# Performance work log

Hardware: AMD Instinct MI355X
Metric: run time of the kernel (lower is better)

## Reference

```python
import jax, jax.numpy as jnp
import numpy as np

N = 1024      # num_nodes
E = 4096      # edges (before self-loops)
HEADS = 8
B = 32
T = 64
HL = 512      # lstm_hidden_size (LSTMCell)
HR = 64       # hid_dim_lstmrr (rainfall LSTM)


def setup_inputs() -> dict:
    key = jax.random.key(0)
    ks = jax.random.split(key, 20)
    rn = lambda i, shape, s=0.05: (jax.random.normal(ks[i], shape, jnp.float32) * s)
    return dict(
        rainfall=rn(0, (B, T, 1), 1.0),
        inflow=rn(1, (B, T, 1), 1.0),
        edge_index=jax.random.randint(ks[2], (2, E), 0, N),
        lstm_Wih=rn(3, (4 * HR, 1)), lstm_Whh=rn(4, (4 * HR, HR)),
        lstm_bih=jnp.zeros(4 * HR), lstm_bhh=jnp.zeros(4 * HR),
        fc_W=rn(5, (N, HR)), fc_b=jnp.zeros(N),
        g1_W=rn(6, (3, HEADS * 3)), g1_as=rn(7, (HEADS, 3)), g1_ad=rn(8, (HEADS, 3)), g1_b=jnp.zeros(HEADS * 3),
        g2_W=rn(9, (24, HEADS * 2)), g2_as=rn(10, (HEADS, 2)), g2_ad=rn(11, (HEADS, 2)), g2_b=jnp.zeros(2),
        cell_Wih=rn(12, (4 * HL, 2 * N)), cell_Whh=rn(13, (4 * HL, HL)),
        cell_bih=jnp.zeros(4 * HL), cell_bhh=jnp.zeros(4 * HL),
        ln_g=jnp.ones(HL), ln_b=jnp.zeros(HL),
        lin_W=rn(14, (2 * N, HL)), lin_b=jnp.zeros(2 * N),
    )


def _gat(h_in, W, a_s, a_d, bias, src, dst, heads, oc, concat):
    # PyG GATConv: shared lin for src/dst, per-head attention, edge softmax by dst.
    n = h_in.shape[0]
    h = (h_in @ W).reshape(n, heads, oc)                       # [N, H, oc]
    logit = jax.nn.leaky_relu(jnp.sum(h * a_s, -1)[src] + jnp.sum(h * a_d, -1)[dst], 0.2)  # [Etot, H]
    m = jax.ops.segment_max(logit, dst, num_segments=n)
    e = jnp.exp(logit - m[dst])
    denom = jax.ops.segment_sum(e, dst, num_segments=n)
    alpha = e / (denom[dst] + 1e-16)                           # [Etot, H]
    out = jax.ops.segment_sum(h[src] * alpha[:, :, None], dst, num_segments=n)
    out = out.reshape(n, heads * oc) if concat else out.mean(1)
    return out + bias, alpha


def reference(rainfall, inflow, lstm_Wih, lstm_Whh, lstm_bih, lstm_bhh, fc_W, fc_b,
              g1_W, g1_as, g1_ad, g1_b, g2_W, g2_as, g2_ad, g2_b,
              cell_Wih, cell_Whh, cell_bih, cell_bhh, ln_g, ln_b, lin_W, lin_b, edge_index):
    Bb, Tt, _ = rainfall.shape
    loops = jnp.arange(N, dtype=edge_index.dtype)
    src = jnp.concatenate([edge_index[0], loops])              # PyG adds self-loops
    dst = jnp.concatenate([edge_index[1], loops])

    # rainfall LSTM (batch_first), gates ordered i,f,g,o as in torch
    def lstm_step(carry, xt):
        h, c = carry
        g = xt @ lstm_Wih.T + h @ lstm_Whh.T + lstm_bih + lstm_bhh
        i, f, gg, o = jnp.split(g, 4, -1)
        c = jax.nn.sigmoid(f) * c + jax.nn.sigmoid(i) * jnp.tanh(gg)
        h = jax.nn.sigmoid(o) * jnp.tanh(c)
        return (h, c), h
    z = jnp.zeros((Bb, HR), rainfall.dtype)
    _, hs = jax.lax.scan(lstm_step, (z, z), rainfall.transpose(1, 0, 2))   # [T, B, HR]
    runoff = jax.nn.leaky_relu(hs @ fc_W.T + fc_b, 0.01)                   # [T, B, N]
    runoff = runoff.at[:, :, 753].add(inflow.transpose(1, 0, 2)[:, :, 0])

    gat1 = jax.vmap(lambda x: _gat(x, g1_W, g1_as, g1_ad, g1_b, src, dst, HEADS, 3, True))
    gat2 = jax.vmap(lambda x: _gat(x, g2_W, g2_as, g2_ad, g2_b, src, dst, HEADS, 2, False))

    def step(carry, r_t):
        hn, cn, xn = carry
        lateral = r_t[:, :, None]                              # [B, N, 1]
        x = jnp.concatenate([xn, lateral], -1)                 # [B, N, 3]
        x1, att = gat1(x)
        x1 = jax.nn.leaky_relu(x1, 0.01)
        x2, _ = gat2(x1)
        x2 = jax.nn.leaky_relu(x2, 0.01)
        xf = x2.reshape(Bb, 2 * N)
        g = xf @ cell_Wih.T + hn @ cell_Whh.T + cell_bih + cell_bhh
        i, f, gg, o = jnp.split(g, 4, -1)
        cn = jax.nn.sigmoid(f) * cn + jax.nn.sigmoid(i) * jnp.tanh(gg)
        hn = jax.nn.sigmoid(o) * jnp.tanh(cn)
        mu = hn.mean(-1, keepdims=True)
        var = ((hn - mu) ** 2).mean(-1, keepdims=True)
        hn = (hn - mu) / jnp.sqrt(var + 1e-5) * ln_g + ln_b
        xn_flat = jax.nn.softplus(hn @ lin_W.T + lin_b)        # [B, 2N]
        return (hn, cn, xn_flat.reshape(Bb, N, 2)), (xn_flat, lateral, att)

    hn0 = jnp.zeros((Bb, HL), rainfall.dtype)
    cn0 = jnp.zeros((Bb, HL), rainfall.dtype)
    xn0 = jnp.zeros((Bb, N, 2), rainfall.dtype)
    _, (pred, lat, att) = jax.lax.scan(step, (hn0, cn0, xn0), runoff)
    prediction = pred.transpose(1, 0, 2)                       # [B, T, 2N]
    Lateral = lat.transpose(1, 0, 2, 3)                        # [B, T, N, 1]
    return prediction, Lateral, att                            # att: [T, B, E+N, HEADS]
```

## Files before the change

### kernel.cpp

```cpp
#include <hip/hip_runtime.h>
#include <hip/hip_bf16.h>

#define BB 32
#define TT 64
#define NNODE 1024
#define EE 4096
#define NEDGE 5120
#define NHEAD 8
#define HLL 512
#define HRR 64
#define TWO_N 2048
#define KCELL 2560

__device__ __forceinline__ float sigmoidf_(float x){ return 1.f/(1.f+expf(-x)); }
__device__ __forceinline__ float leaky(float x, float s){ return x>0.f? x : s*x; }

__global__ __launch_bounds__(256) void k_lstm(
    const float* __restrict__ rain, const float* __restrict__ Wih,
    const float* __restrict__ Whh, const float* __restrict__ bih,
    const float* __restrict__ bhh, float* __restrict__ hs){
  int b = blockIdx.x;
  int j = threadIdx.x;
  __shared__ float h_lds[HRR];
  __shared__ float g_lds[4*HRR];
  float wh[HRR];
  #pragma unroll
  for(int k=0;k<HRR;k++) wh[k] = Whh[j*HRR+k];
  float wi = Wih[j];
  float bias = bih[j] + bhh[j];
  float c = 0.f;
  if(j < HRR) h_lds[j] = 0.f;
  __syncthreads();
  for(int t=0;t<TT;t++){
    float x = rain[b*TT+t];
    float g = fmaf(wi, x, bias);
    #pragma unroll
    for(int k=0;k<HRR;k++) g = fmaf(wh[k], h_lds[k], g);
    g_lds[j] = g;
    __syncthreads();
    if(j < HRR){
      c = sigmoidf_(g_lds[HRR+j])*c + sigmoidf_(g_lds[j])*tanhf(g_lds[2*HRR+j]);
      float h = sigmoidf_(g_lds[3*HRR+j])*tanhf(c);
      h_lds[j] = h;
      hs[(t*BB+b)*HRR + j] = h;
    }
    __syncthreads();
  }
}

__global__ __launch_bounds__(256) void k_runoff(
    const float* __restrict__ hs, const float* __restrict__ fcW,
    const float* __restrict__ fcb, const float* __restrict__ inflow,
    float* __restrict__ runoff, float* __restrict__ lat){
  int p = blockIdx.x;
  int q = p & 3; int tb = p >> 2; int t = tb >> 5; int b = tb & 31;
  int n = q*256 + threadIdx.x;
  __shared__ float hrow[HRR];
  if(threadIdx.x < HRR) hrow[threadIdx.x] = hs[(t*BB+b)*HRR + threadIdx.x];
  __syncthreads();
  const float* wrow = fcW + n*HRR;
  float a0=0.f,a1=0.f,a2=0.f,a3=0.f;
  #pragma unroll
  for(int k=0;k<HRR;k+=4){
    float4 w = *reinterpret_cast<const float4*>(wrow + k);
    a0 = fmaf(w.x, hrow[k+0], a0);
    a1 = fmaf(w.y, hrow[k+1], a1);
    a2 = fmaf(w.z, hrow[k+2], a2);
    a3 = fmaf(w.w, hrow[k+3], a3);
  }
  float acc = (a0+a1)+(a2+a3) + fcb[n];
  float r = leaky(acc, 0.01f);
  if(n == 753) r += inflow[b*TT + t];
  runoff[(t*BB+b)*NNODE + n] = r;
  lat[(size_t)(b*TT+t)*NNODE + n] = r;
}

__global__ __launch_bounds__(1024) void k_csr_off(const int* __restrict__ ei, int* __restrict__ off){
  __shared__ int deg[NNODE];
  __shared__ int scn[NNODE];
  int tid = threadIdx.x;
  deg[tid] = 1;
  __syncthreads();
  for(int e=tid; e<EE; e+=1024) atomicAdd(&deg[ei[EE+e]], 1);
  __syncthreads();
  scn[tid] = deg[tid];
  __syncthreads();
  for(int ofs=1; ofs<1024; ofs<<=1){
    int add = (tid>=ofs)? scn[tid-ofs] : 0;
    __syncthreads();
    scn[tid] += add;
    __syncthreads();
  }
  off[tid+1] = scn[tid];
  if(tid==0) off[0] = 0;
}

__global__ __launch_bounds__(1024) void k_csr_fill(const int* __restrict__ ei,
    const int* __restrict__ off, int* __restrict__ adjp){
  __shared__ int dstb[EE];
  int tid = threadIdx.x;
  for(int e=tid; e<EE; e+=1024) dstb[e] = ei[EE+e];
  __syncthreads();
  int e = blockIdx.x*1024 + tid;
  int myd = dstb[e];
  int rank = 0;
  for(int ep=0; ep<e; ep++) rank += (dstb[ep]==myd) ? 1 : 0;
  adjp[off[myd]+rank] = (ei[e] << 13) | e;
  if(blockIdx.x==0) adjp[off[tid+1]-1] = (tid << 13) | (EE + tid);
}

__global__ __launch_bounds__(256) void k_prep0(const float* __restrict__ runoff,
    const float* __restrict__ g1W, const float* __restrict__ g1as, const float* __restrict__ g1ad,
    float* __restrict__ h1, float* __restrict__ s1, float* __restrict__ d1){
  int idx = blockIdx.x*256 + threadIdx.x;
  int b = idx >> 10; int n = idx & 1023;
  float x2 = runoff[b*NNODE + n];
  float hv[24];
  size_t base = (size_t)b*NNODE + n;
  #pragma unroll
  for(int o=0;o<24;o++){
    hv[o] = x2*g1W[48+o];
    h1[base*24+o] = hv[o];
  }
  #pragma unroll
  for(int hd=0; hd<NHEAD; hd++){
    float s=0.f, d=0.f;
    #pragma unroll
    for(int c=0;c<3;c++){
      float v = hv[hd*3+c];
      s = fmaf(v, g1as[hd*3+c], s);
      d = fmaf(v, g1ad[hd*3+c], d);
    }
    s1[base*8+hd] = s; d1[base*8+hd] = d;
  }
}

__global__ __launch_bounds__(256) void k_gat1f(
    const int* __restrict__ adjp, const int* __restrict__ off,
    const float* __restrict__ h1, const float* __restrict__ s1, const float* __restrict__ d1,
    const float* __restrict__ g1b, const float* __restrict__ g2W,
    const float* __restrict__ g2as, const float* __restrict__ g2ad,
    float* __restrict__ h2, float* __restrict__ s2, float* __restrict__ d2,
    float* __restrict__ att, int t){
  int tid = threadIdx.x;
  int g = tid >> 3; int hd = tid & 7;
  int p = blockIdx.x*32 + g;
  int b = p >> 10; int n = p & 1023;
  __shared__ float ss[NNODE*NHEAD];
  __shared__ float x1buf[32][25];
  size_t bbase = (size_t)b*NNODE;
  for(int i=tid; i<NNODE*NHEAD; i+=256) ss[i] = s1[bbase*8 + i];
  __syncthreads();
  int o0 = off[n], o1 = off[n+1];
  float dn = d1[(bbase+n)*8+hd];
  float m = -1e30f, den = 0.f;
  for(int idx=o0; idx<o1; idx++){
    int pk = adjp[idx]; int s = pk >> 13;
    float lg = leaky(ss[s*8+hd] + dn, 0.2f);
    if(lg > m){ den *= expf(m - lg); m = lg; }
    den += expf(lg - m);
  }
  float inv = 1.f/(den + 1e-16f);
  float o_0=0.f, o_1=0.f, o_2=0.f;
  for(int idx=o0; idx<o1; idx++){
    int pk = adjp[idx]; int s = pk >> 13; int eid = pk & 8191;
    float lg = leaky(ss[s*8+hd] + dn, 0.2f);
    float al = expf(lg - m)*inv;
    att[((size_t)(t*BB+b)*NEDGE + eid)*NHEAD + hd] = al;
    const float* hr = h1 + (bbase+s)*24 + hd*3;
    o_0 = fmaf(hr[0], al, o_0);
    o_1 = fmaf(hr[1], al, o_1);
    o_2 = fmaf(hr[2], al, o_2);
  }
  x1buf[g][hd*3+0] = leaky(o_0 + g1b[hd*3+0], 0.01f);
  x1buf[g][hd*3+1] = leaky(o_1 + g1b[hd*3+1], 0.01f);
  x1buf[g][hd*3+2] = leaky(o_2 + g1b[hd*3+2], 0.01f);
  __syncthreads();
  float h2v0=0.f, h2v1=0.f;
  int oA = hd*2, oB = hd*2+1;
  #pragma unroll
  for(int k=0;k<24;k++){
    float xv = x1buf[g][k];
    h2v0 = fmaf(xv, g2W[k*16+oA], h2v0);
    h2v1 = fmaf(xv, g2W[k*16+oB], h2v1);
  }
  h2[(bbase+n)*16+oA] = h2v0;
  h2[(bbase+n)*16+oB] = h2v1;
  s2[(bbase+n)*8+hd] = h2v0*g2as[oA] + h2v1*g2as[oB];
  d2[(bbase+n)*8+hd] = h2v0*g2ad[oA] + h2v1*g2ad[oB];
}

__global__ __launch_bounds__(256) void k_gat2f(
    const int* __restrict__ adjp, const int* __restrict__ off,
    const float* __restrict__ h2, const float* __restrict__ s2, const float* __restrict__ d2,
    const float* __restrict__ g2b, float* __restrict__ xf){
  int tid = threadIdx.x;
  int g = tid >> 3; int hd = tid & 7;
  int p = blockIdx.x*32 + g;
  int b = p >> 10; int n = p & 1023;
  __shared__ float ss[NNODE*NHEAD];
  __shared__ float outbuf[32][17];
  size_t bbase = (size_t)b*NNODE;
  for(int i=tid; i<NNODE*NHEAD; i+=256) ss[i] = s2[bbase*8 + i];
  __syncthreads();
  int o0 = off[n], o1 = off[n+1];
  float dn = d2[(bbase+n)*8+hd];
  float m = -1e30f, den = 0.f;
  for(int idx=o0; idx<o1; idx++){
    int pk = adjp[idx]; int s = pk >> 13;
    float lg = leaky(ss[s*8+hd] + dn, 0.2f);
    if(lg > m){ den *= expf(m - lg); m = lg; }
    den += expf(lg - m);
  }
  float inv = 1.f/(den + 1e-16f);
  float o_0=0.f, o_1=0.f;
  for(int idx=o0; idx<o1; idx++){
    int pk = adjp[idx]; int s = pk >> 13;
    float lg = leaky(ss[s*8+hd] + dn, 0.2f);
    float al = expf(lg - m)*inv;
    const float* hr = h2 + (bbase+s)*16 + hd*2;
    o_0 = fmaf(hr[0], al, o_0);
    o_1 = fmaf(hr[1], al, o_1);
  }
  outbuf[g][hd*2+0] = o_0;
  outbuf[g][hd*2+1] = o_1;
  __syncthreads();
  if(hd < 2){
    float acc = 0.f;
    #pragma unroll
    for(int k=0;k<8;k++) acc += outbuf[g][k*2+hd];
    float v = leaky(acc*0.125f + g2b[hd], 0.01f);
    xf[b*TWO_N + n*2 + hd] = v;
  }
}

__global__ __launch_bounds__(256) void k_cell_gemm(const float* __restrict__ xf,
    const float* __restrict__ hn, const float* __restrict__ Wih, const float* __restrict__ Whh,
    float* __restrict__ g0, float* __restrict__ g1){
  __shared__ float xl[256*33];
  int bid = blockIdx.x;
  int half = bid >> 8; int jb = bid & 255;
  int tid = threadIdx.x;
  int jl = tid >> 5; int b = tid & 31;
  int j = jb*8 + jl;
  float a0=0.f,a1=0.f,a2=0.f,a3=0.f;
  int kbeg = half*1280, kend = kbeg + 1280;
  for(int k0=kbeg; k0<kend; k0+=256){
    if(k0 < TWO_N){
      for(int i=0;i<32;i++) xl[tid*33+i] = xf[i*TWO_N + k0 + tid];
    } else {
      for(int i=0;i<32;i++) xl[tid*33+i] = hn[i*HLL + (k0-TWO_N) + tid];
    }
    __syncthreads();
    const float* wrow = (k0 < TWO_N) ? (Wih + (size_t)j*TWO_N + k0)
                                     : (Whh + (size_t)j*HLL + (k0-TWO_N));
    #pragma unroll 4
    for(int kk=0; kk<256; kk+=8){
      float4 w0 = *reinterpret_cast<const float4*>(wrow + kk);
      float4 w1 = *reinterpret_cast<const float4*>(wrow + kk + 4);
      const float* xp = &xl[kk*33 + b];
      a0 = fmaf(w0.x, xp[0*33], a0);
      a1 = fmaf(w0.y, xp[1*33], a1);
      a2 = fmaf(w0.z, xp[2*33], a2);
      a3 = fmaf(w0.w, xp[3*33], a3);
      a0 = fmaf(w1.x, xp[4*33], a0);
      a1 = fmaf(w1.y, xp[5*33], a1);
      a2 = fmaf(w1.z, xp[6*33], a2);
      a3 = fmaf(w1.w, xp[7*33], a3);
    }
    __syncthreads();
  }
  float* dst = half ? g1 : g0;
  dst[b*TWO_N + j] = (a0+a1)+(a2+a3);
}

__global__ __launch_bounds__(512) void k_cell_gate(const float* __restrict__ g0,
    const float* __restrict__ g1,
    const float* __restrict__ bih, const float* __restrict__ bhh,
    float* __restrict__ cn, float* __restrict__ hn,
    const float* __restrict__ lng, const float* __restrict__ lnb){
  int b = blockIdx.x; int u = threadIdx.x;
  const float* r0 = g0 + b*TWO_N;
  const float* r1 = g1 + b*TWO_N;
  float gi = r0[u]         + r1[u]         + bih[u]         + bhh[u];
  float gf = r0[HLL+u]     + r1[HLL+u]     + bih[HLL+u]     + bhh[HLL+u];
  float gg = r0[2*HLL+u]   + r1[2*HLL+u]   + bih[2*HLL+u]   + bhh[2*HLL+u];
  float go = r0[3*HLL+u]   + r1[3*HLL+u]   + bih[3*HLL+u]   + bhh[3*HLL+u];
  float c = sigmoidf_(gf)*cn[b*HLL+u] + sigmoidf_(gi)*tanhf(gg);
  cn[b*HLL+u] = c;
  float h = sigmoidf_(go)*tanhf(c);
  __shared__ float red[HLL];
  __shared__ float red2[HLL];
  red[u] = h; red2[u] = h*h;
  __syncthreads();
  for(int s=256; s>0; s>>=1){
    if(u < s){ red[u] += red[u+s]; red2[u] += red2[u+s]; }
    __syncthreads();
  }
  float mu = red[0] * (1.f/HLL);
  float var = red2[0] * (1.f/HLL) - mu*mu;
  float rstd = rsqrtf(var + 1e-5f);
  hn[b*HLL+u] = (h-mu)*rstd*lng[u] + lnb[u];
}

__global__ __launch_bounds__(256) void k_lin(const float* __restrict__ hn,
    const float* __restrict__ W, const float* __restrict__ bias,
    const float* __restrict__ runoff, float* __restrict__ pred,
    float* __restrict__ h1, float* __restrict__ s1, float* __restrict__ d1,
    const float* __restrict__ g1W, const float* __restrict__ g1as, const float* __restrict__ g1ad,
    int t){
  __shared__ float hl[256*33];
  int tid = threadIdx.x;
  int jl = tid >> 5; int b = tid & 31;
  int j = blockIdx.x*8 + jl;
  float a0=0.f,a1=0.f,a2=0.f,a3=0.f;
  for(int k0=0; k0<HLL; k0+=256){
    for(int i=0;i<32;i++) hl[tid*33+i] = hn[i*HLL + k0 + tid];
    __syncthreads();
    const float* wrow = W + (size_t)j*HLL + k0;
    #pragma unroll 4
    for(int kk=0; kk<256; kk+=8){
      float4 w0 = *reinterpret_cast<const float4*>(wrow + kk);
      float4 w1 = *reinterpret_cast<const float4*>(wrow + kk + 4);
      const float* xp = &hl[kk*33 + b];
      a0 = fmaf(w0.x, xp[0*33], a0);
      a1 = fmaf(w0.y, xp[1*33], a1);
      a2 = fmaf(w0.z, xp[2*33], a2);
      a3 = fmaf(w0.w, xp[3*33], a3);
      a0 = fmaf(w1.x, xp[4*33], a0);
      a1 = fmaf(w1.y, xp[5*33], a1);
      a2 = fmaf(w1.z, xp[6*33], a2);
      a3 = fmaf(w1.w, xp[7*33], a3);
    }
    __syncthreads();
  }
  float val = (a0+a1)+(a2+a3) + bias[j];
  float sp = fmaxf(val, 0.f) + log1pf(expf(-fabsf(val)));
  pred[((size_t)b*TT + t)*TWO_N + j] = sp;
  if(t+1 < TT){
    float partner = __shfl_xor(sp, 32);
    if((jl & 1) == 0){
      int n = j >> 1;
      float x2 = runoff[(size_t)(t+1)*BB*NNODE + b*NNODE + n];
      float hv[24];
      size_t base = (size_t)b*NNODE + n;
      #pragma unroll
      for(int o=0;o<24;o++){
        hv[o] = sp*g1W[o] + partner*g1W[24+o] + x2*g1W[48+o];
        h1[base*24+o] = hv[o];
      }
      #pragma unroll
      for(int hd=0; hd<NHEAD; hd++){
        float s=0.f, d=0.f;
        #pragma unroll
        for(int c=0;c<3;c++){
          float v = hv[hd*3+c];
          s = fmaf(v, g1as[hd*3+c], s);
          d = fmaf(v, g1ad[hd*3+c], d);
        }
        s1[base*8+hd] = s; d1[base*8+hd] = d;
      }
    }
  }
}

__global__ __launch_bounds__(512) void k_init(float* __restrict__ hn, float* __restrict__ cn){
  int idx = blockIdx.x*512 + threadIdx.x;
  if(idx < BB*HLL) hn[idx] = 0.f;
  else cn[idx - BB*HLL] = 0.f;
}

extern "C" void kernel_launch(void* const* d_in, const int* in_sizes, int n_in,
                              void* d_out, int out_size, void* d_ws, size_t ws_size,
                              hipStream_t stream){
  const float* rainfall  = (const float*)d_in[0];
  const float* inflow    = (const float*)d_in[1];
  const int*   edge_index= (const int*)  d_in[2];
  const float* lstm_Wih  = (const float*)d_in[3];
  const float* lstm_Whh  = (const float*)d_in[4];
  const float* lstm_bih  = (const float*)d_in[5];
  const float* lstm_bhh  = (const float*)d_in[6];
  const float* fc_W      = (const float*)d_in[7];
  const float* fc_b      = (const float*)d_in[8];
  const float* g1_W      = (const float*)d_in[9];
  const float* g1_as     = (const float*)d_in[10];
  const float* g1_ad     = (const float*)d_in[11];
  const float* g1_b      = (const float*)d_in[12];
  const float* g2_W      = (const float*)d_in[13];
  const float* g2_as     = (const float*)d_in[14];
  const float* g2_ad     = (const float*)d_in[15];
  const float* g2_b      = (const float*)d_in[16];
  const float* cell_Wih  = (const float*)d_in[17];
  const float* cell_Whh  = (const float*)d_in[18];
  const float* cell_bih  = (const float*)d_in[19];
  const float* cell_bhh  = (const float*)d_in[20];
  const float* ln_g      = (const float*)d_in[21];
  const float* ln_b      = (const float*)d_in[22];
  const float* lin_W     = (const float*)d_in[23];
  const float* lin_b     = (const float*)d_in[24];

  float* out  = (float*)d_out;
  float* pred = out;
  float* lat  = out + (size_t)4194304;
  float* att  = out + (size_t)6291456;

  float* ws = (float*)d_ws;
  float* hs     = ws;
  float* runoff = hs + 131072;
  float* h1     = runoff + 2097152;
  float* s1     = h1 + 786432;
  float* d1     = s1 + 262144;
  float* h2     = d1 + 262144;
  float* s2     = h2 + 524288;
  float* d2     = s2 + 262144;
  float* xfb    = d2 + 262144;
  float* g0buf  = xfb + 65536;
  float* g1buf  = g0buf + 65536;
  float* hn     = g1buf + 65536;
  float* cn     = hn + 16384;
  int*   off    = (int*)(cn + 16384);
  int*   adjp   = off + 1032;
  if(ws_size < 19292192ull) return;

  k_init<<<64, 512, 0, stream>>>(hn, cn);
  k_csr_off<<<1, 1024, 0, stream>>>(edge_index, off);
  k_csr_fill<<<4, 1024, 0, stream>>>(edge_index, off, adjp);
  k_lstm<<<BB, 256, 0, stream>>>(rainfall, lstm_Wih, lstm_Whh, lstm_bih, lstm_bhh, hs);
  k_runoff<<<TT*BB*4, 256, 0, stream>>>(hs, fc_W, fc_b, inflow, runoff, lat);
  k_prep0<<<128, 256, 0, stream>>>(runoff, g1_W, g1_as, g1_ad, h1, s1, d1);

  for(int t=0; t<TT; t++){
    k_gat1f<<<1024, 256, 0, stream>>>(adjp, off, h1, s1, d1,
        g1_b, g2_W, g2_as, g2_ad, h2, s2, d2, att, t);
    k_gat2f<<<1024, 256, 0, stream>>>(adjp, off, h2, s2, d2, g2_b, xfb);
    k_cell_gemm<<<512, 256, 0, stream>>>(xfb, hn, cell_Wih, cell_Whh, g0buf, g1buf);
    k_cell_gate<<<BB, 512, 0, stream>>>(g0buf, g1buf, cell_bih, cell_bhh, cn, hn, ln_g, ln_b);
    k_lin<<<256, 256, 0, stream>>>(hn, lin_W, lin_b, runoff, pred,
        h1, s1, d1, g1_W, g1_as, g1_ad, t);
  }
}
```

Baseline: 5.196 ms.

## Fuse both GAT layers into one per-batch kernel with LDS-resident node features

Replaces the separate gat1 and gat2 kernels, the prep kernel and the GAT-input precompute in k_lin with a single kernel that launches one 1024-thread block per batch row. The block keeps node inputs, layer-2 features and attention scores in LDS, recomputes layer-1 projections on the fly from the three raw inputs, and writes attention rows as float4. This removes global round-trips for the h1/s1/d1/h2/s2/d2 intermediates and one launch per timestep. In exchange only 32 blocks run per step, so parallelism across the GPU's compute units drops sharply and each thread handles all heads serially.

```diff
diff --git a/kernel.cpp b/kernel.cpp
--- a/kernel.cpp
+++ b/kernel.cpp
@@ -15,6 +15,40 @@
 __device__ __forceinline__ float sigmoidf_(float x){ return 1.f/(1.f+expf(-x)); }
 __device__ __forceinline__ float leaky(float x, float s){ return x>0.f? x : s*x; }
 
+__global__ __launch_bounds__(1024) void k_csr_off(const int* __restrict__ ei, int* __restrict__ off){
+  __shared__ int deg[NNODE];
+  __shared__ int scn[NNODE];
+  int tid = threadIdx.x;
+  deg[tid] = 1;
+  __syncthreads();
+  for(int e=tid; e<EE; e+=1024) atomicAdd(&deg[ei[EE+e]], 1);
+  __syncthreads();
+  scn[tid] = deg[tid];
+  __syncthreads();
+  for(int ofs=1; ofs<1024; ofs<<=1){
+    int add = (tid>=ofs)? scn[tid-ofs] : 0;
+    __syncthreads();
+    scn[tid] += add;
+    __syncthreads();
+  }
+  off[tid+1] = scn[tid];
+  if(tid==0) off[0] = 0;
+}
+
+__global__ __launch_bounds__(1024) void k_csr_fill(const int* __restrict__ ei,
+    const int* __restrict__ off, int* __restrict__ adjp){
+  __shared__ int dstb[EE];
+  int tid = threadIdx.x;
+  for(int e=tid; e<EE; e+=1024) dstb[e] = ei[EE+e];
+  __syncthreads();
+  int e = blockIdx.x*1024 + tid;
+  int myd = dstb[e];
+  int rank = 0;
+  for(int ep=0; ep<e; ep++) rank += (dstb[ep]==myd) ? 1 : 0;
+  adjp[off[myd]+rank] = (ei[e] << 13) | e;
+  if(blockIdx.x==0) adjp[off[tid+1]-1] = (tid << 13) | (EE + tid);
+}
+
 __global__ __launch_bounds__(256) void k_lstm(
     const float* __restrict__ rain, const float* __restrict__ Wih,
     const float* __restrict__ Whh, const float* __restrict__ bih,
@@ -59,7 +93,7 @@
   if(threadIdx.x < HRR) hrow[threadIdx.x] = hs[(t*BB+b)*HRR + threadIdx.x];
   __syncthreads();
   const float* wrow = fcW + n*HRR;
-  float a0=0.f,a1=0.f,a2=0.f,a3=0.f;
+  float a0=0,a1=0,a2=0,a3=0;
   #pragma unroll
   for(int k=0;k<HRR;k+=4){
     float4 w = *reinterpret_cast<const float4*>(wrow + k);
@@ -75,162 +109,148 @@
   lat[(size_t)(b*TT+t)*NNODE + n] = r;
 }
 
-__global__ __launch_bounds__(1024) void k_csr_off(const int* __restrict__ ei, int* __restrict__ off){
-  __shared__ int deg[NNODE];
-  __shared__ int scn[NNODE];
-  int tid = threadIdx.x;
-  deg[tid] = 1;
-  __syncthreads();
-  for(int e=tid; e<EE; e+=1024) atomicAdd(&deg[ei[EE+e]], 1);
-  __syncthreads();
-  scn[tid] = deg[tid];
-  __syncthreads();
-  for(int ofs=1; ofs<1024; ofs<<=1){
-    int add = (tid>=ofs)? scn[tid-ofs] : 0;
-    __syncthreads();
-    scn[tid] += add;
-    __syncthreads();
-  }
-  off[tid+1] = scn[tid];
-  if(tid==0) off[0] = 0;
-}
-
-__global__ __launch_bounds__(1024) void k_csr_fill(const int* __restrict__ ei,
-    const int* __restrict__ off, int* __restrict__ adjp){
-  __shared__ int dstb[EE];
-  int tid = threadIdx.x;
-  for(int e=tid; e<EE; e+=1024) dstb[e] = ei[EE+e];
-  __syncthreads();
-  int e = blockIdx.x*1024 + tid;
-  int myd = dstb[e];
-  int rank = 0;
-  for(int ep=0; ep<e; ep++) rank += (dstb[ep]==myd) ? 1 : 0;
-  adjp[off[myd]+rank] = (ei[e] << 13) | e;
-  if(blockIdx.x==0) adjp[off[tid+1]-1] = (tid << 13) | (EE + tid);
-}
-
-__global__ __launch_bounds__(256) void k_prep0(const float* __restrict__ runoff,
-    const float* __restrict__ g1W, const float* __restrict__ g1as, const float* __restrict__ g1ad,
-    float* __restrict__ h1, float* __restrict__ s1, float* __restrict__ d1){
-  int idx = blockIdx.x*256 + threadIdx.x;
-  int b = idx >> 10; int n = idx & 1023;
-  float x2 = runoff[b*NNODE + n];
-  float hv[24];
-  size_t base = (size_t)b*NNODE + n;
-  #pragma unroll
-  for(int o=0;o<24;o++){
-    hv[o] = x2*g1W[48+o];
-    h1[base*24+o] = hv[o];
-  }
-  #pragma unroll
-  for(int hd=0; hd<NHEAD; hd++){
-    float s=0.f, d=0.f;
-    #pragma unroll
-    for(int c=0;c<3;c++){
-      float v = hv[hd*3+c];
-      s = fmaf(v, g1as[hd*3+c], s);
-      d = fmaf(v, g1ad[hd*3+c], d);
-    }
-    s1[base*8+hd] = s; d1[base*8+hd] = d;
-  }
-}
-
-__global__ __launch_bounds__(256) void k_gat1f(
+__global__ __launch_bounds__(1024) void k_gat(
     const int* __restrict__ adjp, const int* __restrict__ off,
-    const float* __restrict__ h1, const float* __restrict__ s1, const float* __restrict__ d1,
-    const float* __restrict__ g1b, const float* __restrict__ g2W,
-    const float* __restrict__ g2as, const float* __restrict__ g2ad,
-    float* __restrict__ h2, float* __restrict__ s2, float* __restrict__ d2,
-    float* __restrict__ att, int t){
-  int tid = threadIdx.x;
-  int g = tid >> 3; int hd = tid & 7;
-  int p = blockIdx.x*32 + g;
-  int b = p >> 10; int n = p & 1023;
-  __shared__ float ss[NNODE*NHEAD];
-  __shared__ float x1buf[32][25];
-  size_t bbase = (size_t)b*NNODE;
-  for(int i=tid; i<NNODE*NHEAD; i+=256) ss[i] = s1[bbase*8 + i];
-  __syncthreads();
+    const float* __restrict__ xn, const float* __restrict__ runoff,
+    const float* __restrict__ g1W, const float* __restrict__ g1as,
+    const float* __restrict__ g1ad, const float* __restrict__ g1b,
+    const float* __restrict__ g2W, const float* __restrict__ g2as,
+    const float* __restrict__ g2ad, const float* __restrict__ g2b,
+    float* __restrict__ xf, float* __restrict__ att, int t){
+  __shared__ float SA[NNODE*24];
+  __shared__ float SB[NNODE*8];
+  __shared__ float SC[640];
+  const int tid = threadIdx.x;
+  const int b = blockIdx.x;
+  const int n = tid;
+
+  if(tid < 72)  SC[48+tid]  = g1W[tid];
+  if(tid >= 128 && tid < 512) SC[tid] = g2W[tid-128];
+  if(tid >= 512 && tid < 528) SC[tid] = g2as[tid-512];
+  if(tid >= 528 && tid < 544) SC[tid] = g2ad[tid-528];
+  if(tid >= 544 && tid < 546) SC[tid] = g2b[tid-544];
+  if(tid >= 552 && tid < 576) SC[tid] = g1b[tid-552];
+  if(tid >= 576 && tid < 600){
+    int i = tid-576; int hd = i/3, c = i%3;
+    float s=0,d=0;
+    #pragma unroll
+    for(int cc=0;cc<3;cc++){
+      float w = g1W[c*24+hd*3+cc];
+      s = fmaf(w, g1as[hd*3+cc], s);
+      d = fmaf(w, g1ad[hd*3+cc], d);
+    }
+    SC[i] = s; SC[24+i] = d;
+  }
+  float x0=0.f, x1v=0.f;
+  if(t > 0){ x0 = xn[b*TWO_N+2*n]; x1v = xn[b*TWO_N+2*n+1]; }
+  float x2 = runoff[((size_t)t*BB+b)*NNODE + n];
+  SB[n*3+0]=x0; SB[n*3+1]=x1v; SB[n*3+2]=x2;
+  __syncthreads();
+
   int o0 = off[n], o1 = off[n+1];
-  float dn = d1[(bbase+n)*8+hd];
-  float m = -1e30f, den = 0.f;
-  for(int idx=o0; idx<o1; idx++){
-    int pk = adjp[idx]; int s = pk >> 13;
-    float lg = leaky(ss[s*8+hd] + dn, 0.2f);
-    if(lg > m){ den *= expf(m - lg); m = lg; }
-    den += expf(lg - m);
-  }
-  float inv = 1.f/(den + 1e-16f);
-  float o_0=0.f, o_1=0.f, o_2=0.f;
-  for(int idx=o0; idx<o1; idx++){
-    int pk = adjp[idx]; int s = pk >> 13; int eid = pk & 8191;
-    float lg = leaky(ss[s*8+hd] + dn, 0.2f);
-    float al = expf(lg - m)*inv;
-    att[((size_t)(t*BB+b)*NEDGE + eid)*NHEAD + hd] = al;
-    const float* hr = h1 + (bbase+s)*24 + hd*3;
-    o_0 = fmaf(hr[0], al, o_0);
-    o_1 = fmaf(hr[1], al, o_1);
-    o_2 = fmaf(hr[2], al, o_2);
-  }
-  x1buf[g][hd*3+0] = leaky(o_0 + g1b[hd*3+0], 0.01f);
-  x1buf[g][hd*3+1] = leaky(o_1 + g1b[hd*3+1], 0.01f);
-  x1buf[g][hd*3+2] = leaky(o_2 + g1b[hd*3+2], 0.01f);
-  __syncthreads();
-  float h2v0=0.f, h2v1=0.f;
-  int oA = hd*2, oB = hd*2+1;
+  float m1[8], den1[8], dn1[8];
+  #pragma unroll
+  for(int h=0;h<8;h++){
+    m1[h] = -1e30f; den1[h] = 0.f;
+    dn1[h] = x0*SC[24+h*3+0] + x1v*SC[24+h*3+1] + x2*SC[24+h*3+2];
+  }
+  for(int e=o0;e<o1;e++){
+    int s = adjp[e]>>13;
+    float sx0=SB[s*3], sx1=SB[s*3+1], sx2=SB[s*3+2];
+    #pragma unroll
+    for(int h=0;h<8;h++){
+      float s1 = sx0*SC[h*3+0] + sx1*SC[h*3+1] + sx2*SC[h*3+2];
+      float lg = leaky(s1+dn1[h], 0.2f);
+      if(lg > m1[h]){ den1[h] *= expf(m1[h]-lg); m1[h] = lg; }
+      den1[h] += expf(lg-m1[h]);
+    }
+  }
+  float inv1[8];
+  #pragma unroll
+  for(int h=0;h<8;h++) inv1[h] = 1.f/(den1[h]+1e-16f);
+  float agg[24];
+  #pragma unroll
+  for(int k=0;k<24;k++) agg[k]=0.f;
+  for(int e=o0;e<o1;e++){
+    int pk = adjp[e]; int s = pk>>13; int eid = pk & 8191;
+    float sx0=SB[s*3], sx1=SB[s*3+1], sx2=SB[s*3+2];
+    float at8[8];
+    #pragma unroll
+    for(int h=0;h<8;h++){
+      float s1 = sx0*SC[h*3+0] + sx1*SC[h*3+1] + sx2*SC[h*3+2];
+      float lg = leaky(s1+dn1[h], 0.2f);
+      float al = expf(lg-m1[h])*inv1[h];
+      at8[h] = al;
+      #pragma unroll
+      for(int cc=0;cc<3;cc++){
+        float h1v = sx0*SC[48+h*3+cc] + sx1*SC[48+24+h*3+cc] + sx2*SC[48+48+h*3+cc];
+        agg[h*3+cc] = fmaf(al, h1v, agg[h*3+cc]);
+      }
+    }
+    float* ap = att + ((size_t)(t*BB+b)*NEDGE + eid)*NHEAD;
+    *reinterpret_cast<float4*>(ap)   = make_float4(at8[0],at8[1],at8[2],at8[3]);
+    *reinterpret_cast<float4*>(ap+4) = make_float4(at8[4],at8[5],at8[6],at8[7]);
+  }
+  float x1r[24];
   #pragma unroll
   for(int k=0;k<24;k++){
-    float xv = x1buf[g][k];
-    h2v0 = fmaf(xv, g2W[k*16+oA], h2v0);
-    h2v1 = fmaf(xv, g2W[k*16+oB], h2v1);
-  }
-  h2[(bbase+n)*16+oA] = h2v0;
-  h2[(bbase+n)*16+oB] = h2v1;
-  s2[(bbase+n)*8+hd] = h2v0*g2as[oA] + h2v1*g2as[oB];
-  d2[(bbase+n)*8+hd] = h2v0*g2ad[oA] + h2v1*g2ad[oB];
-}
-
-__global__ __launch_bounds__(256) void k_gat2f(
-    const int* __restrict__ adjp, const int* __restrict__ off,
-    const float* __restrict__ h2, const float* __restrict__ s2, const float* __restrict__ d2,
-    const float* __restrict__ g2b, float* __restrict__ xf){
-  int tid = threadIdx.x;
-  int g = tid >> 3; int hd = tid & 7;
-  int p = blockIdx.x*32 + g;
-  int b = p >> 10; int n = p & 1023;
-  __shared__ float ss[NNODE*NHEAD];
-  __shared__ float outbuf[32][17];
-  size_t bbase = (size_t)b*NNODE;
-  for(int i=tid; i<NNODE*NHEAD; i+=256) ss[i] = s2[bbase*8 + i];
-  __syncthreads();
-  int o0 = off[n], o1 = off[n+1];
-  float dn = d2[(bbase+n)*8+hd];
-  float m = -1e30f, den = 0.f;
-  for(int idx=o0; idx<o1; idx++){
-    int pk = adjp[idx]; int s = pk >> 13;
-    float lg = leaky(ss[s*8+hd] + dn, 0.2f);
-    if(lg > m){ den *= expf(m - lg); m = lg; }
-    den += expf(lg - m);
-  }
-  float inv = 1.f/(den + 1e-16f);
-  float o_0=0.f, o_1=0.f;
-  for(int idx=o0; idx<o1; idx++){
-    int pk = adjp[idx]; int s = pk >> 13;
-    float lg = leaky(ss[s*8+hd] + dn, 0.2f);
-    float al = expf(lg - m)*inv;
-    const float* hr = h2 + (bbase+s)*16 + hd*2;
-    o_0 = fmaf(hr[0], al, o_0);
-    o_1 = fmaf(hr[1], al, o_1);
-  }
-  outbuf[g][hd*2+0] = o_0;
-  outbuf[g][hd*2+1] = o_1;
-  __syncthreads();
-  if(hd < 2){
-    float acc = 0.f;
-    #pragma unroll
-    for(int k=0;k<8;k++) acc += outbuf[g][k*2+hd];
-    float v = leaky(acc*0.125f + g2b[hd], 0.01f);
-    xf[b*TWO_N + n*2 + hd] = v;
+    x1r[k] = leaky(agg[k] + SC[552+k], 0.01f);
+  }
+  __syncthreads();
+
+  float h2r[16];
+  #pragma unroll
+  for(int j=0;j<16;j++) h2r[j]=0.f;
+  #pragma unroll
+  for(int k=0;k<24;k++){
+    float xv = x1r[k];
+    #pragma unroll
+    for(int j=0;j<16;j++) h2r[j] = fmaf(xv, SC[128+k*16+j], h2r[j]);
+  }
+  float d2[8];
+  #pragma unroll
+  for(int h=0;h<8;h++){
+    SB[n*8+h] = h2r[2*h]*SC[512+2*h] + h2r[2*h+1]*SC[512+2*h+1];
+    d2[h]     = h2r[2*h]*SC[528+2*h] + h2r[2*h+1]*SC[528+2*h+1];
+  }
+  #pragma unroll
+  for(int j=0;j<16;j++) SA[n*16+j] = h2r[j];
+  __syncthreads();
+
+  float m2[8], den2[8];
+  #pragma unroll
+  for(int h=0;h<8;h++){ m2[h]=-1e30f; den2[h]=0.f; }
+  for(int e=o0;e<o1;e++){
+    int s = adjp[e]>>13;
+    #pragma unroll
+    for(int h=0;h<8;h++){
+      float lg = leaky(SB[s*8+h]+d2[h], 0.2f);
+      if(lg > m2[h]){ den2[h] *= expf(m2[h]-lg); m2[h] = lg; }
+      den2[h] += expf(lg-m2[h]);
+    }
+  }
+  float inv2[8];
+  #pragma unroll
+  for(int h=0;h<8;h++) inv2[h] = 1.f/(den2[h]+1e-16f);
+  float agg2[16];
+  #pragma unroll
+  for(int j=0;j<16;j++) agg2[j]=0.f;
+  for(int e=o0;e<o1;e++){
+    int s = adjp[e]>>13;
+    #pragma unroll
+    for(int h=0;h<8;h++){
+      float lg = leaky(SB[s*8+h]+d2[h], 0.2f);
+      float al = expf(lg-m2[h])*inv2[h];
+      agg2[2*h]   = fmaf(al, SA[s*16+2*h],   agg2[2*h]);
+      agg2[2*h+1] = fmaf(al, SA[s*16+2*h+1], agg2[2*h+1]);
+    }
+  }
+  #pragma unroll
+  for(int cc=0;cc<2;cc++){
+    float acc=0.f;
+    #pragma unroll
+    for(int h=0;h<8;h++) acc += agg2[2*h+cc];
+    xf[b*TWO_N + n*2 + cc] = leaky(acc*0.125f + SC[544+cc], 0.01f);
   }
 }
 
@@ -259,14 +279,14 @@
       float4 w0 = *reinterpret_cast<const float4*>(wrow + kk);
       float4 w1 = *reinterpret_cast<const float4*>(wrow + kk + 4);
       const float* xp = &xl[kk*33 + b];
-      a0 = fmaf(w0.x, xp[0*33], a0);
-      a1 = fmaf(w0.y, xp[1*33], a1);
-      a2 = fmaf(w0.z, xp[2*33], a2);
-      a3 = fmaf(w0.w, xp[3*33], a3);
-      a0 = fmaf(w1.x, xp[4*33], a0);
-      a1 = fmaf(w1.y, xp[5*33], a1);
-      a2 = fmaf(w1.z, xp[6*33], a2);
-      a3 = fmaf(w1.w, xp[7*33], a3);
+      a0 = fmaf(w0.x, xp[0],   a0);
+      a1 = fmaf(w0.y, xp[33],  a1);
+      a2 = fmaf(w0.z, xp[66],  a2);
+      a3 = fmaf(w0.w, xp[99],  a3);
+      a0 = fmaf(w1.x, xp[132], a0);
+      a1 = fmaf(w1.y, xp[165], a1);
+      a2 = fmaf(w1.z, xp[198], a2);
+      a3 = fmaf(w1.w, xp[231], a3);
     }
     __syncthreads();
   }
@@ -274,7 +294,7 @@
   dst[b*TWO_N + j] = (a0+a1)+(a2+a3);
 }
 
-__global__ __launch_bounds__(512) void k_cell_gate(const float* __restrict__ g0,
+__global__ __launch_bounds__(512) void k_gateln(const float* __restrict__ g0,
     const float* __restrict__ g1,
     const float* __restrict__ bih, const float* __restrict__ bhh,
     float* __restrict__ cn, float* __restrict__ hn,
@@ -282,10 +302,10 @@
   int b = blockIdx.x; int u = threadIdx.x;
   const float* r0 = g0 + b*TWO_N;
   const float* r1 = g1 + b*TWO_N;
-  float gi = r0[u]         + r1[u]         + bih[u]         + bhh[u];
-  float gf = r0[HLL+u]     + r1[HLL+u]     + bih[HLL+u]     + bhh[HLL+u];
-  float gg = r0[2*HLL+u]   + r1[2*HLL+u]   + bih[2*HLL+u]   + bhh[2*HLL+u];
-  float go = r0[3*HLL+u]   + r1[3*HLL+u]   + bih[3*HLL+u]   + bhh[3*HLL+u];
+  float gi = r0[u]       + r1[u]       + bih[u]       + bhh[u];
+  float gf = r0[HLL+u]   + r1[HLL+u]   + bih[HLL+u]   + bhh[HLL+u];
+  float gg = r0[2*HLL+u] + r1[2*HLL+u] + bih[2*HLL+u] + bhh[2*HLL+u];
+  float go = r0[3*HLL+u] + r1[3*HLL+u] + bih[3*HLL+u] + bhh[3*HLL+u];
   float c = sigmoidf_(gf)*cn[b*HLL+u] + sigmoidf_(gi)*tanhf(gg);
   cn[b*HLL+u] = c;
   float h = sigmoidf_(go)*tanhf(c);
@@ -305,10 +325,7 @@
 
 __global__ __launch_bounds__(256) void k_lin(const float* __restrict__ hn,
     const float* __restrict__ W, const float* __restrict__ bias,
-    const float* __restrict__ runoff, float* __restrict__ pred,
-    float* __restrict__ h1, float* __restrict__ s1, float* __restrict__ d1,
-    const float* __restrict__ g1W, const float* __restrict__ g1as, const float* __restrict__ g1ad,
-    int t){
+    float* __restrict__ pred, float* __restrict__ xn, int t){
   __shared__ float hl[256*33];
   int tid = threadIdx.x;
   int jl = tid >> 5; int b = tid & 31;
@@ -323,45 +340,21 @@
       float4 w0 = *reinterpret_cast<const float4*>(wrow + kk);
       float4 w1 = *reinterpret_cast<const float4*>(wrow + kk + 4);
       const float* xp = &hl[kk*33 + b];
-      a0 = fmaf(w0.x, xp[0*33], a0);
-      a1 = fmaf(w0.y, xp[1*33], a1);
-      a2 = fmaf(w0.z, xp[2*33], a2);
-      a3 = fmaf(w0.w, xp[3*33], a3);
-      a0 = fmaf(w1.x, xp[4*33], a0);
-      a1 = fmaf(w1.y, xp[5*33], a1);
-      a2 = fmaf(w1.z, xp[6*33], a2);
-      a3 = fmaf(w1.w, xp[7*33], a3);
+      a0 = fmaf(w0.x, xp[0],   a0);
+      a1 = fmaf(w0.y, xp[33],  a1);
+      a2 = fmaf(w0.z, xp[66],  a2);
+      a3 = fmaf(w0.w, xp[99],  a3);
+      a0 = fmaf(w1.x, xp[132], a0);
+      a1 = fmaf(w1.y, xp[165], a1);
+      a2 = fmaf(w1.z, xp[198], a2);
+      a3 = fmaf(w1.w, xp[231], a3);
     }
     __syncthreads();
   }
   float val = (a0+a1)+(a2+a3) + bias[j];
   float sp = fmaxf(val, 0.f) + log1pf(expf(-fabsf(val)));
   pred[((size_t)b*TT + t)*TWO_N + j] = sp;
-  if(t+1 < TT){
-    float partner = __shfl_xor(sp, 32);
-    if((jl & 1) == 0){
-      int n = j >> 1;
-      float x2 = runoff[(size_t)(t+1)*BB*NNODE + b*NNODE + n];
-      float hv[24];
-      size_t base = (size_t)b*NNODE + n;
-      #pragma unroll
-      for(int o=0;o<24;o++){
-        hv[o] = sp*g1W[o] + partner*g1W[24+o] + x2*g1W[48+o];
-        h1[base*24+o] = hv[o];
-      }
-      #pragma unroll
-      for(int hd=0; hd<NHEAD; hd++){
-        float s=0.f, d=0.f;
-        #pragma unroll
-        for(int c=0;c<3;c++){
-          float v = hv[hd*3+c];
-          s = fmaf(v, g1as[hd*3+c], s);
-          d = fmaf(v, g1ad[hd*3+c], d);
-        }
-        s1[base*8+hd] = s; d1[base*8+hd] = d;
-      }
-    }
-  }
+  xn[b*TWO_N + j] = sp;
 }
 
 __global__ __launch_bounds__(512) void k_init(float* __restrict__ hn, float* __restrict__ cn){
@@ -407,35 +400,27 @@
   float* ws = (float*)d_ws;
   float* hs     = ws;
   float* runoff = hs + 131072;
-  float* h1     = runoff + 2097152;
-  float* s1     = h1 + 786432;
-  float* d1     = s1 + 262144;
-  float* h2     = d1 + 262144;
-  float* s2     = h2 + 524288;
-  float* d2     = s2 + 262144;
-  float* xfb    = d2 + 262144;
+  float* xnb    = runoff + 2097152;
+  float* xfb    = xnb + 65536;
   float* g0buf  = xfb + 65536;
   float* g1buf  = g0buf + 65536;
   float* hn     = g1buf + 65536;
   float* cn     = hn + 16384;
   int*   off    = (int*)(cn + 16384);
   int*   adjp   = off + 1032;
-  if(ws_size < 19292192ull) return;
+  if(ws_size < 10117152ull) return;
 
   k_init<<<64, 512, 0, stream>>>(hn, cn);
   k_csr_off<<<1, 1024, 0, stream>>>(edge_index, off);
   k_csr_fill<<<4, 1024, 0, stream>>>(edge_index, off, adjp);
   k_lstm<<<BB, 256, 0, stream>>>(rainfall, lstm_Wih, lstm_Whh, lstm_bih, lstm_bhh, hs);
   k_runoff<<<TT*BB*4, 256, 0, stream>>>(hs, fc_W, fc_b, inflow, runoff, lat);
-  k_prep0<<<128, 256, 0, stream>>>(runoff, g1_W, g1_as, g1_ad, h1, s1, d1);
 
   for(int t=0; t<TT; t++){
-    k_gat1f<<<1024, 256, 0, stream>>>(adjp, off, h1, s1, d1,
-        g1_b, g2_W, g2_as, g2_ad, h2, s2, d2, att, t);
-    k_gat2f<<<1024, 256, 0, stream>>>(adjp, off, h2, s2, d2, g2_b, xfb);
+    k_gat<<<BB, 1024, 0, stream>>>(adjp, off, xnb, runoff,
+        g1_W, g1_as, g1_ad, g1_b, g2_W, g2_as, g2_ad, g2_b, xfb, att, t);
     k_cell_gemm<<<512, 256, 0, stream>>>(xfb, hn, cell_Wih, cell_Whh, g0buf, g1buf);
-    k_cell_gate<<<BB, 512, 0, stream>>>(g0buf, g1buf, cell_bih, cell_bhh, cn, hn, ln_g, ln_b);
-    k_lin<<<256, 256, 0, stream>>>(hn, lin_W, lin_b, runoff, pred,
-        h1, s1, d1, g1_W, g1_as, g1_ad, t);
-  }
-}
+    k_gateln<<<BB, 512, 0, stream>>>(g0buf, g1buf, cell_bih, cell_bhh, cn, hn, ln_g, ln_b);
+    k_lin<<<256, 256, 0, stream>>>(hn, lin_W, lin_b, pred, xnb, t);
+  }
+}
```

New measurement: 11.20 ms. 2.16x slower.

## Fuse LSTM cell gates into GEMM and LayerNorm into output linear

Applied to the files above, without the earlier changes.

Merges the split-K cell GEMM and the gate kernel into one kernel that arranges each block's rows so it owns all four gates for two units, emitting raw hidden values and partial LayerNorm sums. The output linear kernel then reduces those partial stats and normalizes on the fly while staging its input, also writing hn. This removes one launch per step and the intermediate gate buffers. The cost is half as many GEMM blocks, each running the full K, and a redundant stats reduction in every linear block.

```diff
diff --git a/kernel.cpp b/kernel.cpp
--- a/kernel.cpp
+++ b/kernel.cpp
@@ -14,6 +14,40 @@
 
 __device__ __forceinline__ float sigmoidf_(float x){ return 1.f/(1.f+expf(-x)); }
 __device__ __forceinline__ float leaky(float x, float s){ return x>0.f? x : s*x; }
+
+__global__ __launch_bounds__(1024) void k_csr_off(const int* __restrict__ ei, int* __restrict__ off){
+  __shared__ int deg[NNODE];
+  __shared__ int scn[NNODE];
+  int tid = threadIdx.x;
+  deg[tid] = 1;
+  __syncthreads();
+  for(int e=tid; e<EE; e+=1024) atomicAdd(&deg[ei[EE+e]], 1);
+  __syncthreads();
+  scn[tid] = deg[tid];
+  __syncthreads();
+  for(int ofs=1; ofs<1024; ofs<<=1){
+    int add = (tid>=ofs)? scn[tid-ofs] : 0;
+    __syncthreads();
+    scn[tid] += add;
+    __syncthreads();
+  }
+  off[tid+1] = scn[tid];
+  if(tid==0) off[0] = 0;
+}
+
+__global__ __launch_bounds__(1024) void k_csr_fill(const int* __restrict__ ei,
+    const int* __restrict__ off, int* __restrict__ adjp){
+  __shared__ int dstb[EE];
+  int tid = threadIdx.x;
+  for(int e=tid; e<EE; e+=1024) dstb[e] = ei[EE+e];
+  __syncthreads();
+  int e = blockIdx.x*1024 + tid;
+  int myd = dstb[e];
+  int rank = 0;
+  for(int ep=0; ep<e; ep++) rank += (dstb[ep]==myd) ? 1 : 0;
+  adjp[off[myd]+rank] = (ei[e] << 13) | e;
+  if(blockIdx.x==0) adjp[off[tid+1]-1] = (tid << 13) | (EE + tid);
+}
 
 __global__ __launch_bounds__(256) void k_lstm(
     const float* __restrict__ rain, const float* __restrict__ Wih,
@@ -59,7 +93,7 @@
   if(threadIdx.x < HRR) hrow[threadIdx.x] = hs[(t*BB+b)*HRR + threadIdx.x];
   __syncthreads();
   const float* wrow = fcW + n*HRR;
-  float a0=0.f,a1=0.f,a2=0.f,a3=0.f;
+  float a0=0,a1=0,a2=0,a3=0;
   #pragma unroll
   for(int k=0;k<HRR;k+=4){
     float4 w = *reinterpret_cast<const float4*>(wrow + k);
@@ -73,40 +107,6 @@
   if(n == 753) r += inflow[b*TT + t];
   runoff[(t*BB+b)*NNODE + n] = r;
   lat[(size_t)(b*TT+t)*NNODE + n] = r;
-}
-
-__global__ __launch_bounds__(1024) void k_csr_off(const int* __restrict__ ei, int* __restrict__ off){
-  __shared__ int deg[NNODE];
-  __shared__ int scn[NNODE];
-  int tid = threadIdx.x;
-  deg[tid] = 1;
-  __syncthreads();
-  for(int e=tid; e<EE; e+=1024) atomicAdd(&deg[ei[EE+e]], 1);
-  __syncthreads();
-  scn[tid] = deg[tid];
-  __syncthreads();
-  for(int ofs=1; ofs<1024; ofs<<=1){
-    int add = (tid>=ofs)? scn[tid-ofs] : 0;
-    __syncthreads();
-    scn[tid] += add;
-    __syncthreads();
-  }
-  off[tid+1] = scn[tid];
-  if(tid==0) off[0] = 0;
-}
-
-__global__ __launch_bounds__(1024) void k_csr_fill(const int* __restrict__ ei,
-    const int* __restrict__ off, int* __restrict__ adjp){
-  __shared__ int dstb[EE];
-  int tid = threadIdx.x;
-  for(int e=tid; e<EE; e+=1024) dstb[e] = ei[EE+e];
-  __syncthreads();
-  int e = blockIdx.x*1024 + tid;
-  int myd = dstb[e];
-  int rank = 0;
-  for(int ep=0; ep<e; ep++) rank += (dstb[ep]==myd) ? 1 : 0;
-  adjp[off[myd]+rank] = (ei[e] << 13) | e;
-  if(blockIdx.x==0) adjp[off[tid+1]-1] = (tid << 13) | (EE + tid);
 }
 
 __global__ __launch_bounds__(256) void k_prep0(const float* __restrict__ runoff,
@@ -234,18 +234,18 @@
   }
 }
 
-__global__ __launch_bounds__(256) void k_cell_gemm(const float* __restrict__ xf,
+__global__ __launch_bounds__(256) void k_cellgate(const float* __restrict__ xf,
     const float* __restrict__ hn, const float* __restrict__ Wih, const float* __restrict__ Whh,
-    float* __restrict__ g0, float* __restrict__ g1){
+    const float* __restrict__ bih, const float* __restrict__ bhh,
+    float* __restrict__ cn, float* __restrict__ hraw, float* __restrict__ stats){
   __shared__ float xl[256*33];
-  int bid = blockIdx.x;
-  int half = bid >> 8; int jb = bid & 255;
-  int tid = threadIdx.x;
-  int jl = tid >> 5; int b = tid & 31;
-  int j = jb*8 + jl;
-  float a0=0.f,a1=0.f,a2=0.f,a3=0.f;
-  int kbeg = half*1280, kend = kbeg + 1280;
-  for(int k0=kbeg; k0<kend; k0+=256){
+  const int q = blockIdx.x;
+  const int tid = threadIdx.x;
+  const int jl = tid >> 5;
+  const int b  = tid & 31;
+  const int j  = (jl>>1)*512 + q*2 + (jl&1);
+  float a0=0,a1=0,a2=0,a3=0;
+  for(int k0=0; k0<KCELL; k0+=256){
     if(k0 < TWO_N){
       for(int i=0;i<32;i++) xl[tid*33+i] = xf[i*TWO_N + k0 + tid];
     } else {
@@ -259,63 +259,92 @@
       float4 w0 = *reinterpret_cast<const float4*>(wrow + kk);
       float4 w1 = *reinterpret_cast<const float4*>(wrow + kk + 4);
       const float* xp = &xl[kk*33 + b];
-      a0 = fmaf(w0.x, xp[0*33], a0);
-      a1 = fmaf(w0.y, xp[1*33], a1);
-      a2 = fmaf(w0.z, xp[2*33], a2);
-      a3 = fmaf(w0.w, xp[3*33], a3);
-      a0 = fmaf(w1.x, xp[4*33], a0);
-      a1 = fmaf(w1.y, xp[5*33], a1);
-      a2 = fmaf(w1.z, xp[6*33], a2);
-      a3 = fmaf(w1.w, xp[7*33], a3);
-    }
-    __syncthreads();
-  }
-  float* dst = half ? g1 : g0;
-  dst[b*TWO_N + j] = (a0+a1)+(a2+a3);
-}
-
-__global__ __launch_bounds__(512) void k_cell_gate(const float* __restrict__ g0,
-    const float* __restrict__ g1,
-    const float* __restrict__ bih, const float* __restrict__ bhh,
-    float* __restrict__ cn, float* __restrict__ hn,
-    const float* __restrict__ lng, const float* __restrict__ lnb){
-  int b = blockIdx.x; int u = threadIdx.x;
-  const float* r0 = g0 + b*TWO_N;
-  const float* r1 = g1 + b*TWO_N;
-  float gi = r0[u]         + r1[u]         + bih[u]         + bhh[u];
-  float gf = r0[HLL+u]     + r1[HLL+u]     + bih[HLL+u]     + bhh[HLL+u];
-  float gg = r0[2*HLL+u]   + r1[2*HLL+u]   + bih[2*HLL+u]   + bhh[2*HLL+u];
-  float go = r0[3*HLL+u]   + r1[3*HLL+u]   + bih[3*HLL+u]   + bhh[3*HLL+u];
-  float c = sigmoidf_(gf)*cn[b*HLL+u] + sigmoidf_(gi)*tanhf(gg);
-  cn[b*HLL+u] = c;
-  float h = sigmoidf_(go)*tanhf(c);
-  __shared__ float red[HLL];
-  __shared__ float red2[HLL];
-  red[u] = h; red2[u] = h*h;
-  __syncthreads();
-  for(int s=256; s>0; s>>=1){
-    if(u < s){ red[u] += red[u+s]; red2[u] += red2[u+s]; }
-    __syncthreads();
-  }
-  float mu = red[0] * (1.f/HLL);
-  float var = red2[0] * (1.f/HLL) - mu*mu;
-  float rstd = rsqrtf(var + 1e-5f);
-  hn[b*HLL+u] = (h-mu)*rstd*lng[u] + lnb[u];
-}
-
-__global__ __launch_bounds__(256) void k_lin(const float* __restrict__ hn,
+      a0 = fmaf(w0.x, xp[0],   a0);
+      a1 = fmaf(w0.y, xp[33],  a1);
+      a2 = fmaf(w0.z, xp[66],  a2);
+      a3 = fmaf(w0.w, xp[99],  a3);
+      a0 = fmaf(w1.x, xp[132], a0);
+      a1 = fmaf(w1.y, xp[165], a1);
+      a2 = fmaf(w1.z, xp[198], a2);
+      a3 = fmaf(w1.w, xp[231], a3);
+    }
+    __syncthreads();
+  }
+  float gv = (a0+a1)+(a2+a3) + bih[j] + bhh[j];
+  xl[jl*32 + b] = gv;
+  __syncthreads();
+  float hval = 0.f;
+  if(jl < 2){
+    int u = q*2 + jl;
+    float gi = xl[(0+jl)*32 + b];
+    float gf = xl[(2+jl)*32 + b];
+    float gg = xl[(4+jl)*32 + b];
+    float go = xl[(6+jl)*32 + b];
+    float c = sigmoidf_(gf)*cn[b*HLL+u] + sigmoidf_(gi)*tanhf(gg);
+    cn[b*HLL+u] = c;
+    hval = sigmoidf_(go)*tanhf(c);
+    hraw[b*HLL+u] = hval;
+  }
+  __syncthreads();
+  if(jl < 2){
+    xl[256 + jl*32 + b] = hval;
+    xl[384 + jl*32 + b] = hval*hval;
+  }
+  __syncthreads();
+  if(jl == 0){
+    stats[(q*32 + b)*2 + 0] = xl[256 + b] + xl[288 + b];
+    stats[(q*32 + b)*2 + 1] = xl[384 + b] + xl[416 + b];
+  }
+}
+
+__global__ __launch_bounds__(256) void k_linln(const float* __restrict__ hraw,
+    const float* __restrict__ stats, const float* __restrict__ lng, const float* __restrict__ lnb,
+    float* __restrict__ hn,
     const float* __restrict__ W, const float* __restrict__ bias,
     const float* __restrict__ runoff, float* __restrict__ pred,
     float* __restrict__ h1, float* __restrict__ s1, float* __restrict__ d1,
     const float* __restrict__ g1W, const float* __restrict__ g1as, const float* __restrict__ g1ad,
     int t){
   __shared__ float hl[256*33];
-  int tid = threadIdx.x;
+  __shared__ float red1[256], red2[256];
+  __shared__ float musd[32], rstds[32];
+  const int q = blockIdx.x;
+  const int tid = threadIdx.x;
+  {
+    int b8 = tid >> 3, l8 = tid & 7;
+    float s = 0.f, s2 = 0.f;
+    for(int qq = l8*32; qq < l8*32+32; qq++){
+      s  += stats[(qq*32 + b8)*2 + 0];
+      s2 += stats[(qq*32 + b8)*2 + 1];
+    }
+    red1[tid] = s; red2[tid] = s2;
+    __syncthreads();
+    if(l8 < 4){ red1[tid] += red1[tid+4]; red2[tid] += red2[tid+4]; }
+    __syncthreads();
+    if(l8 < 2){ red1[tid] += red1[tid+2]; red2[tid] += red2[tid+2]; }
+    __syncthreads();
+    if(l8 == 0){
+      float S = red1[tid] + red1[tid+1];
+      float S2 = red2[tid] + red2[tid+1];
+      float mu = S * (1.f/HLL);
+      float var = S2 * (1.f/HLL) - mu*mu;
+      musd[b8] = mu;
+      rstds[b8] = rsqrtf(var + 1e-5f);
+    }
+    __syncthreads();
+  }
+  if(tid < 64){
+    int e = q*64 + tid; int b = e >> 9; int u = e & 511;
+    hn[e] = (hraw[e] - musd[b])*rstds[b]*lng[u] + lnb[u];
+  }
   int jl = tid >> 5; int b = tid & 31;
-  int j = blockIdx.x*8 + jl;
+  int j = q*8 + jl;
   float a0=0.f,a1=0.f,a2=0.f,a3=0.f;
   for(int k0=0; k0<HLL; k0+=256){
-    for(int i=0;i<32;i++) hl[tid*33+i] = hn[i*HLL + k0 + tid];
+    float lg_ = lng[k0+tid], lb_ = lnb[k0+tid];
+    __syncthreads();
+    for(int i=0;i<32;i++)
+      hl[tid*33+i] = (hraw[i*HLL + k0 + tid] - musd[i])*rstds[i]*lg_ + lb_;
     __syncthreads();
     const float* wrow = W + (size_t)j*HLL + k0;
     #pragma unroll 4
@@ -323,16 +352,15 @@
       float4 w0 = *reinterpret_cast<const float4*>(wrow + kk);
       float4 w1 = *reinterpret_cast<const float4*>(wrow + kk + 4);
       const float* xp = &hl[kk*33 + b];
-      a0 = fmaf(w0.x, xp[0*33], a0);
-      a1 = fmaf(w0.y, xp[1*33], a1);
-      a2 = fmaf(w0.z, xp[2*33], a2);
-      a3 = fmaf(w0.w, xp[3*33], a3);
-      a0 = fmaf(w1.x, xp[4*33], a0);
-      a1 = fmaf(w1.y, xp[5*33], a1);
-      a2 = fmaf(w1.z, xp[6*33], a2);
-      a3 = fmaf(w1.w, xp[7*33], a3);
-    }
-    __syncthreads();
+      a0 = fmaf(w0.x, xp[0],   a0);
+      a1 = fmaf(w0.y, xp[33],  a1);
+      a2 = fmaf(w0.z, xp[66],  a2);
+      a3 = fmaf(w0.w, xp[99],  a3);
+      a0 = fmaf(w1.x, xp[132], a0);
+      a1 = fmaf(w1.y, xp[165], a1);
+      a2 = fmaf(w1.z, xp[198], a2);
+      a3 = fmaf(w1.w, xp[231], a3);
+    }
   }
   float val = (a0+a1)+(a2+a3) + bias[j];
   float sp = fmaxf(val, 0.f) + log1pf(expf(-fabsf(val)));
@@ -342,21 +370,21 @@
     if((jl & 1) == 0){
       int n = j >> 1;
       float x2 = runoff[(size_t)(t+1)*BB*NNODE + b*NNODE + n];
-      float hv[24];
+      float hv2[24];
       size_t base = (size_t)b*NNODE + n;
       #pragma unroll
       for(int o=0;o<24;o++){
-        hv[o] = sp*g1W[o] + partner*g1W[24+o] + x2*g1W[48+o];
-        h1[base*24+o] = hv[o];
+        hv2[o] = sp*g1W[o] + partner*g1W[24+o] + x2*g1W[48+o];
+        h1[base*24+o] = hv2[o];
       }
       #pragma unroll
       for(int hd=0; hd<NHEAD; hd++){
         float s=0.f, d=0.f;
         #pragma unroll
-        for(int c=0;c<3;c++){
-          float v = hv[hd*3+c];
-          s = fmaf(v, g1as[hd*3+c], s);
-          d = fmaf(v, g1ad[hd*3+c], d);
+        for(int c2=0;c2<3;c2++){
+          float v2 = hv2[hd*3+c2];
+          s = fmaf(v2, g1as[hd*3+c2], s);
+          d = fmaf(v2, g1ad[hd*3+c2], d);
         }
         s1[base*8+hd] = s; d1[base*8+hd] = d;
       }
@@ -414,13 +442,13 @@
   float* s2     = h2 + 524288;
   float* d2     = s2 + 262144;
   float* xfb    = d2 + 262144;
-  float* g0buf  = xfb + 65536;
-  float* g1buf  = g0buf + 65536;
-  float* hn     = g1buf + 65536;
+  float* hraw   = xfb + 65536;
+  float* stats  = hraw + 16384;
+  float* hn     = stats + 16384;
   float* cn     = hn + 16384;
   int*   off    = (int*)(cn + 16384);
   int*   adjp   = off + 1032;
-  if(ws_size < 19292192ull) return;
+  if(ws_size < 18898976ull) return;
 
   k_init<<<64, 512, 0, stream>>>(hn, cn);
   k_csr_off<<<1, 1024, 0, stream>>>(edge_index, off);
@@ -433,9 +461,9 @@
     k_gat1f<<<1024, 256, 0, stream>>>(adjp, off, h1, s1, d1,
         g1_b, g2_W, g2_as, g2_ad, h2, s2, d2, att, t);
     k_gat2f<<<1024, 256, 0, stream>>>(adjp, off, h2, s2, d2, g2_b, xfb);
-    k_cell_gemm<<<512, 256, 0, stream>>>(xfb, hn, cell_Wih, cell_Whh, g0buf, g1buf);
-    k_cell_gate<<<BB, 512, 0, stream>>>(g0buf, g1buf, cell_bih, cell_bhh, cn, hn, ln_g, ln_b);
-    k_lin<<<256, 256, 0, stream>>>(hn, lin_W, lin_b, runoff, pred,
-        h1, s1, d1, g1_W, g1_as, g1_ad, t);
-  }
-}
+    k_cellgate<<<256, 256, 0, stream>>>(xfb, hn, cell_Wih, cell_Whh,
+        cell_bih, cell_bhh, cn, hraw, stats);
+    k_linln<<<256, 256, 0, stream>>>(hraw, stats, ln_g, ln_b, hn,
+        lin_W, lin_b, runoff, pred, h1, s1, d1, g1_W, g1_as, g1_ad, t);
+  }
+}
```

Result: slower. 6.363 ms (+22.5%).
